# Optimization experiments

Hardware: AMD Instinct MI355X
Metric: run time of the kernel (lower is better)

## Reference

```python
import math
import jax, jax.numpy as jnp
import numpy as np

EPS = 1e-8

def setup_inputs() -> dict:
    key = jax.random.key(0)
    k1, k2, k3, k4 = jax.random.split(key, 4)
    B, Cin, Cout, K, S, H, W = 8, 512, 512, 3, 512, 64, 64
    return {
        "x": jax.random.normal(k1, (B, Cin, H, W), dtype=jnp.float32),
        "style": jax.random.normal(k2, (B, S), dtype=jnp.float32),
        "weight": jax.random.normal(k3, (1, Cout, Cin, K, K), dtype=jnp.float32),
        "mod_weight": jax.random.normal(k4, (Cin, S), dtype=jnp.float32),
        "mod_bias": jnp.ones((Cin,), dtype=jnp.float32),
    }


def reference(x, style, weight, mod_weight, mod_bias):
    B, Cin, H, W = x.shape
    _, Cout, _, K, _ = weight.shape
    S = mod_weight.shape[1]
    lin_scale = 1.0 / math.sqrt(S)          # EqualLinear scale (lr_mul=1)
    conv_scale = 1.0 / math.sqrt(Cin * K * K)  # fan_in scale
    pad = K // 2

    # modulation: EqualLinear(style) -> [B, Cin], reshaped to [B,1,Cin,1,1]
    s = style @ (mod_weight * lin_scale).T + mod_bias
    s5 = s[:, None, :, None, None]

    # per-sample modulated weight [B, Cout, Cin, K, K]
    w = conv_scale * weight * s5
    demod = jax.lax.rsqrt(jnp.sum(w * w, axis=(2, 3, 4)) + EPS)  # [B, Cout]
    w = w * demod[:, :, None, None, None]

    # batch-as-groups conv: x -> [1, B*Cin, H, W], w -> [B*Cout, Cin, K, K]
    xg = x.reshape(1, B * Cin, H, W)
    wg = w.reshape(B * Cout, Cin, K, K)
    out = jax.lax.conv_general_dilated(
        xg, wg,
        window_strides=(1, 1),
        padding=[(pad, pad), (pad, pad)],
        dimension_numbers=("NCHW", "OIHW", "NCHW"),
        feature_group_count=B,
    )
    out = out.reshape(B, Cout, H, W)
    return out, s5
```

## Files before the change

kernel.cpp:

```cpp
#include <hip/hip_runtime.h>
#include <hip/hip_bf16.h>


typedef __attribute__((ext_vector_type(8))) short short8;
typedef __attribute__((ext_vector_type(4))) float f32x4;

#define LIN_SCALE 0.04419417382415922f
#define CONV_SCALE 0.014731391274719739f
#define CONV_SCALE2 (1.0f/4608.0f)
#define OUT_IMG (8*512*64*64)

static __device__ __forceinline__ unsigned short f2bf(float f) {
    union { float f; unsigned int u; } a; a.f = f;
    unsigned int u = a.u;
    return (unsigned short)((u + 0x7fffu + ((u >> 16) & 1u)) >> 16);
}
static __device__ __forceinline__ short8 as_s8(uint4 v) {
    union { uint4 u; short8 s; } x; x.u = v; return x.s;
}

__global__ __launch_bounds__(256) void k_style(const float* __restrict__ style,
                                               const float* __restrict__ mw,
                                               const float* __restrict__ mb,
                                               float* __restrict__ s_ws,
                                               float* __restrict__ out_s5) {
    int wid = blockIdx.x * 4 + (threadIdx.x >> 6);
    int lane = threadIdx.x & 63;
    int b = wid >> 9, ci = wid & 511;
    float sum = 0.f;
    for (int k = lane; k < 512; k += 64)
        sum += style[b*512 + k] * mw[ci*512 + k];
    for (int off = 32; off > 0; off >>= 1) sum += __shfl_xor(sum, off);
    if (lane == 0) {
        float v = sum * LIN_SCALE + mb[ci];
        s_ws[b*512 + ci] = v;
        out_s5[b*512 + ci] = v;
    }
}

__global__ __launch_bounds__(256) void k_wprep(const float* __restrict__ weight,
                                               unsigned short* __restrict__ wfrag) {
    __shared__ float wsh[4608];
    int co = blockIdx.x;
    int cog = co >> 4, l15 = co & 15;
    for (int i = threadIdx.x; i < 4608; i += 256) wsh[i] = weight[co*4608 + i];
    __syncthreads();
    uint4* wf4 = (uint4*)wfrag;
    for (int idx = threadIdx.x; idx < 576; idx += 256) {
        int t = idx / 64;
        int rem = idx & 63;
        int cig = rem >> 2, lg = rem & 3;
        union { unsigned short h[8]; uint4 v; } u;
        #pragma unroll
        for (int j = 0; j < 8; ++j)
            u.h[j] = f2bf(wsh[(cig*32 + lg*8 + j)*9 + t] * CONV_SCALE);
        wf4[((t*16 + cig)*32 + cog)*64 + lg*16 + l15] = u.v;
    }
}

__global__ __launch_bounds__(256) void k_demod(const float* __restrict__ weight,
                                               const float* __restrict__ s_ws,
                                               float* __restrict__ demod) {
    __shared__ float s2[4096];
    __shared__ float red[4][8];
    int co = blockIdx.x;
    for (int i = threadIdx.x; i < 4096; i += 256) { float v = s_ws[i]; s2[i] = v*v; }
    __syncthreads();
    float acc[8] = {0,0,0,0,0,0,0,0};
    for (int idx = threadIdx.x; idx < 4608; idx += 256) {
        float w = weight[co*4608 + idx];
        float w2 = w*w;
        int ci = idx / 9;
        #pragma unroll
        for (int b = 0; b < 8; ++b) acc[b] += w2 * s2[b*512 + ci];
    }
    int lane = threadIdx.x & 63, wv = threadIdx.x >> 6;
    #pragma unroll
    for (int b = 0; b < 8; ++b) {
        float v = acc[b];
        for (int off = 32; off > 0; off >>= 1) v += __shfl_xor(v, off);
        if (lane == 0) red[wv][b] = v;
    }
    __syncthreads();
    if (threadIdx.x < 8) {
        float t = red[0][threadIdx.x] + red[1][threadIdx.x]
                + red[2][threadIdx.x] + red[3][threadIdx.x];
        demod[threadIdx.x*512 + co] = rsqrtf(t * CONV_SCALE2 + 1e-8f);
    }
}

__global__ __launch_bounds__(256) void k_xprep(const float* __restrict__ x,
                                               const float* __restrict__ s_ws,
                                               unsigned short* __restrict__ xs) {
    __shared__ unsigned short tile[32 * 520];
    int w0 = blockIdx.x * 32, h = blockIdx.y, b = blockIdx.z;
    int t = threadIdx.x;
    int wl = t & 31, cih = t >> 5;
    for (int ci0 = 0; ci0 < 512; ci0 += 8) {
        int ci = ci0 + cih;
        float sv = s_ws[b*512 + ci];
        float v = x[((b*512 + ci)*64 + h)*64 + (w0 + wl)] * sv;
        tile[wl*520 + ci] = f2bf(v);
    }
    __syncthreads();
    int lane = t & 63, wv = t >> 6;
    const uint4* t4 = (const uint4*)tile;
    uint4* xs4 = (uint4*)xs;
    for (int w = wv; w < 32; w += 4) {
        uint4 v = t4[w*65 + lane];
        xs4[((b*64 + h)*64 + (w0 + w))*64 + lane] = v;
    }
}

__global__ __launch_bounds__(256) void k_conv(const unsigned short* __restrict__ xs,
                                              const unsigned short* __restrict__ wfrag,
                                              const float* __restrict__ demod,
                                              float* __restrict__ out) {
    __shared__ uint4 lds[2][1056];
    int cot = blockIdx.x;
    int r0  = blockIdx.y * 2;
    int b   = blockIdx.z;
    int tid = threadIdx.x;
    int lane = tid & 63, wid = tid >> 6;
    int wm = wid & 1, wn = wid >> 1;
    int l15 = lane & 15, lg = lane >> 4;
    int cobase = cot*128 + wm*64;
    int cog0 = cobase >> 4;

    const uint4* xs4 = (const uint4*)xs;
    const uint4* wf4 = (const uint4*)wfrag;

    f32x4 acc[4][4];
    #pragma unroll
    for (int i = 0; i < 4; ++i)
        #pragma unroll
        for (int j = 0; j < 4; ++j) acc[i][j] = (f32x4){0.f,0.f,0.f,0.f};

    auto stage = [&](int p, int cq) {
        for (int idx = tid; idx < 1056; idx += 256) {
            int g = idx & 3;
            int pair = idx >> 2;
            int c = pair % 66;
            int r = pair / 66;
            int rin = r0 - 1 + r;
            int cin = c - 1;
            uint4 v = {0u,0u,0u,0u};
            if (((unsigned)rin < 64u) && ((unsigned)cin < 64u))
                v = xs4[((b*64 + rin)*64 + cin)*64 + cq + g];
            lds[p][(r*4 + g)*66 + c] = v;
        }
    };

    stage(0, 0);
    __syncthreads();

    #pragma unroll 1
    for (int step = 0; step < 16; ++step) {
        int p = step & 1;
        if (step < 15) stage(p ^ 1, (step+1) * 4);
        #pragma unroll
        for (int kh = 0; kh < 3; ++kh) {
            int rt = wn + kh;
            #pragma unroll
            for (int kw = 0; kw < 3; ++kw) {
                int t = kh*3 + kw;
                short8 a[4], bx[4];
                #pragma unroll
                for (int mf = 0; mf < 4; ++mf)
                    a[mf] = as_s8(wf4[((t*16 + step)*32 + cog0 + mf)*64 + lane]);
                #pragma unroll
                for (int nf = 0; nf < 4; ++nf) {
                    int slot = (rt*4 + lg)*66 + nf*16 + kw + l15;
                    bx[nf] = as_s8(lds[p][slot]);
                }
                #pragma unroll
                for (int mf = 0; mf < 4; ++mf)
                    #pragma unroll
                    for (int nf = 0; nf < 4; ++nf)
                        acc[mf][nf] = __builtin_amdgcn_mfma_f32_16x16x32_bf16(
                            a[mf], bx[nf], acc[mf][nf], 0, 0, 0);
            }
        }
        __syncthreads();
    }

    int r = r0 + wn;
    const float* dmp = demod + b*512;
    #pragma unroll
    for (int mf = 0; mf < 4; ++mf) {
        #pragma unroll
        for (int reg = 0; reg < 4; ++reg) {
            int co = cobase + mf*16 + lg*4 + reg;
            float dm = dmp[co];
            #pragma unroll
            for (int nf = 0; nf < 4; ++nf) {
                int c = nf*16 + l15;
                out[((b*512 + co)*64 + r)*64 + c] = acc[mf][nf][reg] * dm;
            }
        }
    }
}

extern "C" void kernel_launch(void* const* d_in, const int* in_sizes, int n_in,
                              void* d_out, int out_size, void* d_ws, size_t ws_size,
                              hipStream_t stream) {
    const float* x      = (const float*)d_in[0];
    const float* style  = (const float*)d_in[1];
    const float* weight = (const float*)d_in[2];
    const float* mw     = (const float*)d_in[3];
    const float* mb     = (const float*)d_in[4];
    float* out = (float*)d_out;

    float* s_ws           = (float*)d_ws;
    float* demod_ws       = (float*)((char*)d_ws + 16384);
    unsigned short* wfrag = (unsigned short*)((char*)d_ws + 32768);
    unsigned short* xs    = (unsigned short*)((char*)d_ws + 4751360);

    k_style<<<1024, 256, 0, stream>>>(style, mw, mb, s_ws, out + OUT_IMG);
    k_wprep<<<512, 256, 0, stream>>>(weight, wfrag);
    k_demod<<<512, 256, 0, stream>>>(weight, s_ws, demod_ws);
    k_xprep<<<dim3(2, 64, 8), 256, 0, stream>>>(x, s_ws, xs);
    k_conv<<<dim3(4, 32, 8), 256, 0, stream>>>(xs, wfrag, demod_ws, out);
}
```

Before: 329.3 us.

## Double conv output-channel tile per block, swizzle block order, unroll staging loop

Each conv block now computes 256 output channels instead of 128, doubling the accumulator tiles per wave (8x4 MFMA tiles), so each staged input tile in LDS is reused across twice as many channels and input staging traffic halves. The grid becomes a 1D launch of 512 blocks with a remapping that interleaves batches across consecutive block IDs, likely to spread work across XCDs and improve L2 locality. The LDS staging loop is rewritten with precomputed indices and a fixed unroll to avoid per-element div/mod. The larger accumulator raises register pressure (launch_bounds 256,2) and halves the block count, which may reduce occupancy.

New measurement: 682.7 us. 107% more time.

```diff
diff --git a/kernel.cpp b/kernel.cpp
--- a/kernel.cpp
+++ b/kernel.cpp
@@ -112,42 +112,48 @@
     }
 }
 
-__global__ __launch_bounds__(256) void k_conv(const unsigned short* __restrict__ xs,
-                                              const unsigned short* __restrict__ wfrag,
-                                              const float* __restrict__ demod,
-                                              float* __restrict__ out) {
+__global__ __launch_bounds__(256, 2) void k_conv(const unsigned short* __restrict__ xs,
+                                                 const unsigned short* __restrict__ wfrag,
+                                                 const float* __restrict__ demod,
+                                                 float* __restrict__ out) {
     __shared__ uint4 lds[2][1056];
-    int cot = blockIdx.x;
-    int r0  = blockIdx.y * 2;
-    int b   = blockIdx.z;
+    int orig = ((blockIdx.x & 7) << 6) + (blockIdx.x >> 3);
+    int b   = orig >> 6;
+    int rem = orig & 63;
+    int r0  = (rem >> 1) * 2;
+    int cot = rem & 1;
     int tid = threadIdx.x;
     int lane = tid & 63, wid = tid >> 6;
     int wm = wid & 1, wn = wid >> 1;
     int l15 = lane & 15, lg = lane >> 4;
-    int cobase = cot*128 + wm*64;
+    int cobase = cot*256 + wm*128;
     int cog0 = cobase >> 4;
 
     const uint4* xs4 = (const uint4*)xs;
     const uint4* wf4 = (const uint4*)wfrag;
 
-    f32x4 acc[4][4];
+    f32x4 acc[8][4];
     #pragma unroll
-    for (int i = 0; i < 4; ++i)
+    for (int i = 0; i < 8; ++i)
         #pragma unroll
         for (int j = 0; j < 4; ++j) acc[i][j] = (f32x4){0.f,0.f,0.f,0.f};
 
+    int sg = tid & 3;
+    int sc0 = tid >> 2;
     auto stage = [&](int p, int cq) {
-        for (int idx = tid; idx < 1056; idx += 256) {
-            int g = idx & 3;
-            int pair = idx >> 2;
-            int c = pair % 66;
-            int r = pair / 66;
-            int rin = r0 - 1 + r;
-            int cin = c - 1;
-            uint4 v = {0u,0u,0u,0u};
-            if (((unsigned)rin < 64u) && ((unsigned)cin < 64u))
-                v = xs4[((b*64 + rin)*64 + cin)*64 + cq + g];
-            lds[p][(r*4 + g)*66 + c] = v;
+        int c = sc0, r = 0;
+        #pragma unroll
+        for (int k = 0; k < 5; ++k) {
+            if (k < 4 || tid < 32) {
+                int rin = r0 - 1 + r;
+                int cin = c - 1;
+                uint4 v = {0u,0u,0u,0u};
+                if (((unsigned)rin < 64u) && ((unsigned)cin < 64u))
+                    v = xs4[((b*64 + rin)*64 + cin)*64 + cq + sg];
+                lds[p][(r*4 + sg)*66 + c] = v;
+            }
+            c += 64;
+            if (c >= 66) { c -= 66; ++r; }
         }
     };
 
@@ -164,9 +170,9 @@
             #pragma unroll
             for (int kw = 0; kw < 3; ++kw) {
                 int t = kh*3 + kw;
-                short8 a[4], bx[4];
+                short8 a[8], bx[4];
                 #pragma unroll
-                for (int mf = 0; mf < 4; ++mf)
+                for (int mf = 0; mf < 8; ++mf)
                     a[mf] = as_s8(wf4[((t*16 + step)*32 + cog0 + mf)*64 + lane]);
                 #pragma unroll
                 for (int nf = 0; nf < 4; ++nf) {
@@ -174,7 +180,7 @@
                     bx[nf] = as_s8(lds[p][slot]);
                 }
                 #pragma unroll
-                for (int mf = 0; mf < 4; ++mf)
+                for (int mf = 0; mf < 8; ++mf)
                     #pragma unroll
                     for (int nf = 0; nf < 4; ++nf)
                         acc[mf][nf] = __builtin_amdgcn_mfma_f32_16x16x32_bf16(
@@ -187,7 +193,7 @@
     int r = r0 + wn;
     const float* dmp = demod + b*512;
     #pragma unroll
-    for (int mf = 0; mf < 4; ++mf) {
+    for (int mf = 0; mf < 8; ++mf) {
         #pragma unroll
         for (int reg = 0; reg < 4; ++reg) {
             int co = cobase + mf*16 + lg*4 + reg;
@@ -220,5 +226,5 @@
     k_wprep<<<512, 256, 0, stream>>>(weight, wfrag);
     k_demod<<<512, 256, 0, stream>>>(weight, s_ws, demod_ws);
     k_xprep<<<dim3(2, 64, 8), 256, 0, stream>>>(x, s_ws, xs);
-    k_conv<<<dim3(4, 32, 8), 256, 0, stream>>>(xs, wfrag, demod_ws, out);
-}
+    k_conv<<<512, 256, 0, stream>>>(xs, wfrag, demod_ws, out);
+}
```

## Stage conv input through registers into single LDS buffer with occupancy hint

Applied to the files above, without the earlier changes.

Replaces the double-buffered LDS staging in the conv kernel with register prefetch. Each thread loads its next four input rows into registers while the current step computes, then writes them into a single LDS buffer between two barriers. Padding columns are zeroed once up front, the per-element div/mod index math is gone, and launch_bounds now asks for 4 blocks per CU. This halves LDS use and cuts staging address arithmetic, but adds a second barrier per step and more register pressure under the occupancy cap.

Measured after the change: 353.6 us. 1.07x slower.

```diff
diff --git a/kernel.cpp b/kernel.cpp
--- a/kernel.cpp
+++ b/kernel.cpp
@@ -112,11 +112,11 @@
     }
 }
 
-__global__ __launch_bounds__(256) void k_conv(const unsigned short* __restrict__ xs,
-                                              const unsigned short* __restrict__ wfrag,
-                                              const float* __restrict__ demod,
-                                              float* __restrict__ out) {
-    __shared__ uint4 lds[2][1056];
+__global__ __launch_bounds__(256, 4) void k_conv(const unsigned short* __restrict__ xs,
+                                                 const unsigned short* __restrict__ wfrag,
+                                                 const float* __restrict__ demod,
+                                                 float* __restrict__ out) {
+    __shared__ uint4 lds[1056];
     int cot = blockIdx.x;
     int r0  = blockIdx.y * 2;
     int b   = blockIdx.z;
@@ -136,28 +136,37 @@
         #pragma unroll
         for (int j = 0; j < 4; ++j) acc[i][j] = (f32x4){0.f,0.f,0.f,0.f};
 
-    auto stage = [&](int p, int cq) {
-        for (int idx = tid; idx < 1056; idx += 256) {
-            int g = idx & 3;
-            int pair = idx >> 2;
-            int c = pair % 66;
-            int r = pair / 66;
-            int rin = r0 - 1 + r;
-            int cin = c - 1;
-            uint4 v = {0u,0u,0u,0u};
-            if (((unsigned)rin < 64u) && ((unsigned)cin < 64u))
-                v = xs4[((b*64 + rin)*64 + cin)*64 + cq + g];
-            lds[p][(r*4 + g)*66 + c] = v;
+    int sg  = tid & 3;
+    int sc  = 1 + (tid >> 2);
+    int scm1 = tid >> 2;
+    const uint4* xrow = xs4 + ((b*64 + (r0 - 1))*64 + scm1)*64 + sg;
+
+    uint4 st[4];
+    auto issue = [&](int cq) {
+        #pragma unroll
+        for (int k = 0; k < 4; ++k) {
+            int rin = r0 - 1 + k;
+            st[k] = (uint4){0u,0u,0u,0u};
+            if ((unsigned)rin < 64u) st[k] = xrow[k*4096 + cq];
         }
     };
 
-    stage(0, 0);
-    __syncthreads();
+    if (tid < 32) {
+        int q = tid & 15;
+        int col = (tid >> 4) ? 65 : 0;
+        lds[q*66 + col] = (uint4){0u,0u,0u,0u};
+    }
+    issue(0);
 
     #pragma unroll 1
     for (int step = 0; step < 16; ++step) {
-        int p = step & 1;
-        if (step < 15) stage(p ^ 1, (step+1) * 4);
+        __syncthreads();
+        #pragma unroll
+        for (int k = 0; k < 4; ++k)
+            lds[(k*4 + sg)*66 + sc] = st[k];
+        __syncthreads();
+        if (step < 15) issue((step+1) * 4);
+
         #pragma unroll
         for (int kh = 0; kh < 3; ++kh) {
             int rt = wn + kh;
@@ -166,13 +175,13 @@
                 int t = kh*3 + kw;
                 short8 a[4], bx[4];
                 #pragma unroll
+                for (int nf = 0; nf < 4; ++nf) {
+                    int slot = (rt*4 + lg)*66 + nf*16 + kw + l15;
+                    bx[nf] = as_s8(lds[slot]);
+                }
+                #pragma unroll
                 for (int mf = 0; mf < 4; ++mf)
                     a[mf] = as_s8(wf4[((t*16 + step)*32 + cog0 + mf)*64 + lane]);
-                #pragma unroll
-                for (int nf = 0; nf < 4; ++nf) {
-                    int slot = (rt*4 + lg)*66 + nf*16 + kw + l15;
-                    bx[nf] = as_s8(lds[p][slot]);
-                }
                 #pragma unroll
                 for (int mf = 0; mf < 4; ++mf)
                     #pragma unroll
@@ -181,7 +190,6 @@
                             a[mf], bx[nf], acc[mf][nf], 0, 0, 0);
             }
         }
-        __syncthreads();
     }
 
     int r = r0 + wn;
```
